# Performance work log

Measured on AMD Instinct MI355X. Metric: run time of the kernel, lower is better.

Reference implementation:

```python
import jax, jax.numpy as jnp
import numpy as np

B, T, ENC, DEC, ATTN = 64, 2048, 512, 512, 256


def setup_inputs() -> dict:
    key = jax.random.key(0)
    k1, k2, k3, k4, k5, k6 = jax.random.split(key, 6)
    enc_out = jax.random.normal(k1, (B, T, ENC), dtype=jnp.float32)
    dec_hidden = jax.random.normal(k2, (B, DEC), dtype=jnp.float32)
    mask = jax.random.randint(k3, (B, T), 0, 2) == 1  # True = masked out
    # learned params (Linear with bias=False); torch Linear weight is [out,in],
    # we store transposed [in,out] for x @ W convention
    s_enc = 1.0 / np.sqrt(ENC)
    s_dec = 1.0 / np.sqrt(DEC)
    s_v = 1.0 / np.sqrt(ATTN)
    W_enc = jax.random.uniform(k4, (ENC, ATTN), jnp.float32, -s_enc, s_enc)
    W_dec = jax.random.uniform(k5, (DEC, ATTN), jnp.float32, -s_dec, s_dec)
    v = jax.random.uniform(k6, (ATTN,), jnp.float32, -s_v, s_v)
    return {"enc_out": enc_out, "dec_hidden": dec_hidden, "mask": mask,
            "W_enc": W_enc, "W_dec": W_dec, "v": v}


def reference(enc_out, dec_hidden, mask, W_enc, W_dec, v):
    # proj_enc: [B,T,A]; proj_dec: [B,1,A]
    proj_enc = jnp.einsum('bte,ea->bta', enc_out, W_enc)
    proj_dec = jnp.einsum('bd,da->ba', dec_hidden, W_dec)[:, None, :]
    # energy: [B,T] -- additive (Bahdanau) score
    energy = jnp.einsum('bta,a->bt', jnp.tanh(proj_enc + proj_dec), v)
    energy = jnp.where(mask, -jnp.inf, energy)
    attn_w = jax.nn.softmax(energy, axis=-1)
    attn_w = jnp.nan_to_num(attn_w, nan=0.0)  # fully-masked rows -> 0
    context = jnp.einsum('bt,bte->be', attn_w, enc_out)
    return context, attn_w
```

## Files before the change

### kernel.cpp

```cpp
#include <hip/hip_runtime.h>
#include <stdint.h>

#define Bx 64
#define Tx 2048
#define ENCx 512
#define ATTx 256

typedef float f4 __attribute__((ext_vector_type(4)));
typedef float f32x4 __attribute__((ext_vector_type(4)));
typedef short bf16x8 __attribute__((ext_vector_type(8)));

__device__ __forceinline__ unsigned short f2bf(float f) {
  union { float f; uint32_t u; } c; c.f = f;
  uint32_t u = c.u;
  u += 0x7fffu + ((u >> 16) & 1u);
  return (unsigned short)(u >> 16);
}

__device__ __forceinline__ float ftanh(float x) {
  x = fminf(8.f, fmaxf(-8.f, x));
  float z = __expf(2.f * x);
  return 1.f - __fdividef(2.f, z + 1.f);
}

__global__ void k0_wt(const float* __restrict__ W, unsigned short* __restrict__ WTc) {
  int tid = blockIdx.x * 256 + threadIdx.x;
  int kc = tid >> 13;
  int r = tid & 8191;
  int n = r >> 5;
  int kk = r & 31;
  WTc[tid] = f2bf(W[(kc * 32 + kk) * ATTx + n]);
}

__global__ void k1_pd(const float* __restrict__ dec, const float* __restrict__ Wd,
                      float* __restrict__ pd) {
  __shared__ float ld[512];
  int b = blockIdx.x, a = threadIdx.x;
  ld[a] = dec[b * 512 + a];
  ld[a + 256] = dec[b * 512 + a + 256];
  __syncthreads();
  float s = 0.f;
#pragma unroll 8
  for (int d = 0; d < 512; ++d) s = fmaf(ld[d], Wd[d * ATTx + a], s);
  pd[b * ATTx + a] = s;
}

__global__ __launch_bounds__(256) void k2_energy(
    const float* __restrict__ enc, const unsigned short* __restrict__ WTc,
    const float* __restrict__ pd, const float* __restrict__ v,
    const int* __restrict__ mask, float* __restrict__ energy) {
  __shared__ unsigned short Alds[64 * 40];
  __shared__ unsigned short Wlds[256 * 40];
  __shared__ float ep[4][64];

  const int tid = threadIdx.x;
  const int wid = tid >> 6;
  const int lane = tid & 63;
  const int q = lane >> 4;
  const int c15 = lane & 15;
  const int m0 = blockIdx.x * 64;
  const int b = m0 >> 11;

  f32x4 acc[4][4];
#pragma unroll
  for (int i = 0; i < 4; ++i)
#pragma unroll
    for (int j = 0; j < 4; ++j) { f32x4 z = {0.f,0.f,0.f,0.f}; acc[i][j] = z; }

  const int ar = tid >> 2;
  const int ak = (tid & 3) * 8;
  const int wn = tid >> 2;
  const int wk = (tid & 3) * 8;

  for (int kc = 0; kc < 16; ++kc) {
    const f4* ap = (const f4*)(enc + (size_t)(m0 + ar) * ENCx + kc * 32 + ak);
    f4 a0 = ap[0];
    f4 a1 = ap[1];
    uint4 wv[4];
    const uint4* wp = (const uint4*)(WTc + kc * 8192);
#pragma unroll
    for (int it = 0; it < 4; ++it) wv[it] = wp[it * 256 + tid];

    if (kc) __syncthreads();

    union { unsigned short s[8]; uint4 u; } aw;
    aw.s[0] = f2bf(a0.x); aw.s[1] = f2bf(a0.y); aw.s[2] = f2bf(a0.z); aw.s[3] = f2bf(a0.w);
    aw.s[4] = f2bf(a1.x); aw.s[5] = f2bf(a1.y); aw.s[6] = f2bf(a1.z); aw.s[7] = f2bf(a1.w);
    *(uint4*)&Alds[ar * 40 + ak] = aw.u;
#pragma unroll
    for (int it = 0; it < 4; ++it)
      *(uint4*)&Wlds[(it * 64 + wn) * 40 + wk] = wv[it];
    __syncthreads();

    bf16x8 af[4], bfr[4];
#pragma unroll
    for (int rt = 0; rt < 4; ++rt)
      af[rt] = *(const bf16x8*)&Alds[(rt * 16 + c15) * 40 + q * 8];
#pragma unroll
    for (int ct = 0; ct < 4; ++ct)
      bfr[ct] = *(const bf16x8*)&Wlds[(wid * 64 + ct * 16 + c15) * 40 + q * 8];
#pragma unroll
    for (int rt = 0; rt < 4; ++rt)
#pragma unroll
      for (int ct = 0; ct < 4; ++ct)
        acc[rt][ct] = __builtin_amdgcn_mfma_f32_16x16x32_bf16(af[rt], bfr[ct], acc[rt][ct], 0, 0, 0);
  }

  float part[4][4];
#pragma unroll
  for (int rt = 0; rt < 4; ++rt)
#pragma unroll
    for (int i = 0; i < 4; ++i) part[rt][i] = 0.f;
#pragma unroll
  for (int ct = 0; ct < 4; ++ct) {
    int col = wid * 64 + ct * 16 + c15;
    float pdv = pd[b * ATTx + col];
    float vv = v[col];
#pragma unroll
    for (int rt = 0; rt < 4; ++rt)
#pragma unroll
      for (int i = 0; i < 4; ++i)
        part[rt][i] += ftanh(acc[rt][ct][i] + pdv) * vv;
  }
#pragma unroll
  for (int s = 1; s < 16; s <<= 1)
#pragma unroll
    for (int rt = 0; rt < 4; ++rt)
#pragma unroll
      for (int i = 0; i < 4; ++i)
        part[rt][i] += __shfl_xor(part[rt][i], s, 64);
  if (c15 == 0)
#pragma unroll
    for (int rt = 0; rt < 4; ++rt)
#pragma unroll
      for (int i = 0; i < 4; ++i)
        ep[wid][rt * 16 + q * 4 + i] = part[rt][i];
  __syncthreads();
  if (tid < 64) {
    float e = ep[0][tid] + ep[1][tid] + ep[2][tid] + ep[3][tid];
    int gm = m0 + tid;
    if (mask[gm]) e = -1e30f;
    energy[gm] = e;
  }
}

__global__ void k3_softmax(const float* __restrict__ energy, float* __restrict__ attn) {
  __shared__ float redm[4];
  __shared__ float redl[4];
  int b = blockIdx.x, tid = threadIdx.x;
  int lane = tid & 63, wid = tid >> 6;
  float e[8];
#pragma unroll
  for (int i = 0; i < 8; ++i) e[i] = energy[b * Tx + tid + i * 256];
  float m = e[0];
#pragma unroll
  for (int i = 1; i < 8; ++i) m = fmaxf(m, e[i]);
#pragma unroll
  for (int s = 1; s < 64; s <<= 1) m = fmaxf(m, __shfl_xor(m, s, 64));
  if (lane == 0) redm[wid] = m;
  __syncthreads();
  m = fmaxf(fmaxf(redm[0], redm[1]), fmaxf(redm[2], redm[3]));
  bool dead = (m < -1e29f);
  float w[8];
  float l = 0.f;
#pragma unroll
  for (int i = 0; i < 8; ++i) { w[i] = dead ? 0.f : __expf(e[i] - m); l += w[i]; }
#pragma unroll
  for (int s = 1; s < 64; s <<= 1) l += __shfl_xor(l, s, 64);
  if (lane == 0) redl[wid] = l;
  __syncthreads();
  l = redl[0] + redl[1] + redl[2] + redl[3];
  float inv = dead ? 0.f : __fdividef(1.f, l);
#pragma unroll
  for (int i = 0; i < 8; ++i) attn[b * Tx + tid + i * 256] = w[i] * inv;
}

__global__ void k4_ctx(const float* __restrict__ enc, const float* __restrict__ attn,
                       float* __restrict__ part) {
  __shared__ float wl[256];
  __shared__ f4 comb[128];
  int tc = blockIdx.x & 7, b = blockIdx.x >> 3;
  int tid = threadIdx.x;
  wl[tid] = attn[b * Tx + tc * 256 + tid];
  __syncthreads();
  int tl = tid >> 7;
  int ef = tid & 127;
  f4 a = {0.f, 0.f, 0.f, 0.f};
  const f4* base = (const f4*)(enc + ((size_t)b * Tx + tc * 256) * ENCx) + ef;
  for (int t = tl; t < 256; t += 2) {
    float wv = wl[t];
    f4 x = base[(size_t)t * 128];
    a += x * wv;
  }
  if (tl == 1) comb[ef] = a;
  __syncthreads();
  if (tl == 0) {
    a += comb[ef];
    *((f4*)(part + ((size_t)tc * 64 + b) * 512) + ef) = a;
  }
}

__global__ void k5_red(const float* __restrict__ part, float* __restrict__ ctx) {
  int idx = blockIdx.x * 256 + threadIdx.x;
  float s = 0.f;
#pragma unroll
  for (int tc = 0; tc < 8; ++tc) s += part[tc * 32768 + idx];
  ctx[idx] = s;
}

extern "C" void kernel_launch(void* const* d_in, const int* in_sizes, int n_in,
                              void* d_out, int out_size, void* d_ws, size_t ws_size,
                              hipStream_t stream) {
  const float* enc   = (const float*)d_in[0];
  const float* dec   = (const float*)d_in[1];
  const int*   mask  = (const int*)d_in[2];
  const float* W_enc = (const float*)d_in[3];
  const float* W_dec = (const float*)d_in[4];
  const float* v     = (const float*)d_in[5];
  float* ctx  = (float*)d_out;
  float* attn = ctx + Bx * ENCx;
  char* ws = (char*)d_ws;
  unsigned short* WTc = (unsigned short*)ws;
  float* pd     = (float*)(ws + 262144);
  float* energy = (float*)(ws + 262144 + 65536);
  float* part   = (float*)(ws + 262144 + 65536 + 524288);

  k0_wt<<<512, 256, 0, stream>>>(W_enc, WTc);
  k1_pd<<<64, 256, 0, stream>>>(dec, W_dec, pd);
  k2_energy<<<2048, 256, 0, stream>>>(enc, WTc, pd, v, mask, energy);
  k3_softmax<<<64, 256, 0, stream>>>(energy, attn);
  k4_ctx<<<512, 256, 0, stream>>>(enc, attn, part);
  k5_red<<<128, 256, 0, stream>>>(part, ctx);
}
```

Baseline: 577.9 us.

## Drop LDS staging in energy GEMM and split context reduction finer

The energy kernel now has each wave compute a 32-row by 256-column tile. A and W fragments are loaded straight from global memory into registers, with no LDS staging and no per-k-chunk barriers. It uses a cheaper packed bf16 conversion (round-half-up via perm), keeps pd/v in LDS, and writes masked energies directly without a cross-wave LDS reduction. The context kernel splits T into 16 chunks instead of 8 to launch more blocks, which doubles the partial sums the final reduce has to read. W is re-read from global/L2 by each wave, and the larger accumulator array raises register pressure.

```diff
diff --git a/kernel.cpp b/kernel.cpp
--- a/kernel.cpp
+++ b/kernel.cpp
@@ -15,6 +15,12 @@
   uint32_t u = c.u;
   u += 0x7fffu + ((u >> 16) & 1u);
   return (unsigned short)(u >> 16);
+}
+
+__device__ __forceinline__ uint32_t pk_bf(float lo, float hi) {
+  uint32_t a = __float_as_uint(lo) + 0x8000u;
+  uint32_t b = __float_as_uint(hi) + 0x8000u;
+  return __builtin_amdgcn_perm(b, a, 0x07060302u);
 }
 
 __device__ __forceinline__ float ftanh(float x) {
@@ -49,98 +55,85 @@
     const float* __restrict__ enc, const unsigned short* __restrict__ WTc,
     const float* __restrict__ pd, const float* __restrict__ v,
     const int* __restrict__ mask, float* __restrict__ energy) {
-  __shared__ unsigned short Alds[64 * 40];
-  __shared__ unsigned short Wlds[256 * 40];
-  __shared__ float ep[4][64];
-
+  __shared__ float pdv[256];
+  __shared__ float vvs[256];
   const int tid = threadIdx.x;
   const int wid = tid >> 6;
   const int lane = tid & 63;
   const int q = lane >> 4;
   const int c15 = lane & 15;
-  const int m0 = blockIdx.x * 64;
+  const int m0 = blockIdx.x * 128;
   const int b = m0 >> 11;
 
-  f32x4 acc[4][4];
-#pragma unroll
-  for (int i = 0; i < 4; ++i)
-#pragma unroll
-    for (int j = 0; j < 4; ++j) { f32x4 z = {0.f,0.f,0.f,0.f}; acc[i][j] = z; }
-
-  const int ar = tid >> 2;
-  const int ak = (tid & 3) * 8;
-  const int wn = tid >> 2;
-  const int wk = (tid & 3) * 8;
+  pdv[tid] = pd[b * ATTx + tid];
+  vvs[tid] = v[tid];
+  __syncthreads();
+
+  const int mrow = m0 + wid * 32 + c15;
+  const float* a0p = enc + (size_t)mrow * ENCx + q * 8;
+  const float* a1p = a0p + 16 * ENCx;
+  const unsigned short* wb = WTc + c15 * 32 + q * 8;
+
+  f32x4 acc[2][16];
+#pragma unroll
+  for (int mt = 0; mt < 2; ++mt)
+#pragma unroll
+    for (int ct = 0; ct < 16; ++ct) { f32x4 z = {0.f,0.f,0.f,0.f}; acc[mt][ct] = z; }
 
   for (int kc = 0; kc < 16; ++kc) {
-    const f4* ap = (const f4*)(enc + (size_t)(m0 + ar) * ENCx + kc * 32 + ak);
-    f4 a0 = ap[0];
-    f4 a1 = ap[1];
-    uint4 wv[4];
-    const uint4* wp = (const uint4*)(WTc + kc * 8192);
-#pragma unroll
-    for (int it = 0; it < 4; ++it) wv[it] = wp[it * 256 + tid];
-
-    if (kc) __syncthreads();
-
-    union { unsigned short s[8]; uint4 u; } aw;
-    aw.s[0] = f2bf(a0.x); aw.s[1] = f2bf(a0.y); aw.s[2] = f2bf(a0.z); aw.s[3] = f2bf(a0.w);
-    aw.s[4] = f2bf(a1.x); aw.s[5] = f2bf(a1.y); aw.s[6] = f2bf(a1.z); aw.s[7] = f2bf(a1.w);
-    *(uint4*)&Alds[ar * 40 + ak] = aw.u;
-#pragma unroll
-    for (int it = 0; it < 4; ++it)
-      *(uint4*)&Wlds[(it * 64 + wn) * 40 + wk] = wv[it];
-    __syncthreads();
-
-    bf16x8 af[4], bfr[4];
-#pragma unroll
-    for (int rt = 0; rt < 4; ++rt)
-      af[rt] = *(const bf16x8*)&Alds[(rt * 16 + c15) * 40 + q * 8];
-#pragma unroll
-    for (int ct = 0; ct < 4; ++ct)
-      bfr[ct] = *(const bf16x8*)&Wlds[(wid * 64 + ct * 16 + c15) * 40 + q * 8];
-#pragma unroll
-    for (int rt = 0; rt < 4; ++rt)
-#pragma unroll
-      for (int ct = 0; ct < 4; ++ct)
-        acc[rt][ct] = __builtin_amdgcn_mfma_f32_16x16x32_bf16(af[rt], bfr[ct], acc[rt][ct], 0, 0, 0);
-  }
-
-  float part[4][4];
-#pragma unroll
-  for (int rt = 0; rt < 4; ++rt)
-#pragma unroll
-    for (int i = 0; i < 4; ++i) part[rt][i] = 0.f;
-#pragma unroll
-  for (int ct = 0; ct < 4; ++ct) {
-    int col = wid * 64 + ct * 16 + c15;
-    float pdv = pd[b * ATTx + col];
-    float vv = v[col];
-#pragma unroll
-    for (int rt = 0; rt < 4; ++rt)
+    f4 x0 = *(const f4*)(a0p + kc * 32);
+    f4 x1 = *(const f4*)(a0p + kc * 32 + 4);
+    f4 y0 = *(const f4*)(a1p + kc * 32);
+    f4 y1 = *(const f4*)(a1p + kc * 32 + 4);
+    bf16x8 bfr[16];
+    const unsigned short* wkc = wb + kc * 8192;
+#pragma unroll
+    for (int ct = 0; ct < 16; ++ct)
+      bfr[ct] = *(const bf16x8*)(wkc + ct * 512);
+
+    union { uint32_t u[4]; bf16x8 v; } am0, am1;
+    am0.u[0] = pk_bf(x0.x, x0.y); am0.u[1] = pk_bf(x0.z, x0.w);
+    am0.u[2] = pk_bf(x1.x, x1.y); am0.u[3] = pk_bf(x1.z, x1.w);
+    am1.u[0] = pk_bf(y0.x, y0.y); am1.u[1] = pk_bf(y0.z, y0.w);
+    am1.u[2] = pk_bf(y1.x, y1.y); am1.u[3] = pk_bf(y1.z, y1.w);
+
+#pragma unroll
+    for (int ct = 0; ct < 16; ++ct) {
+      acc[0][ct] = __builtin_amdgcn_mfma_f32_16x16x32_bf16(am0.v, bfr[ct], acc[0][ct], 0, 0, 0);
+      acc[1][ct] = __builtin_amdgcn_mfma_f32_16x16x32_bf16(am1.v, bfr[ct], acc[1][ct], 0, 0, 0);
+    }
+  }
+
+  float ps[2][4];
+#pragma unroll
+  for (int mt = 0; mt < 2; ++mt)
+#pragma unroll
+    for (int i = 0; i < 4; ++i) ps[mt][i] = 0.f;
+#pragma unroll
+  for (int ct = 0; ct < 16; ++ct) {
+    float pv = pdv[ct * 16 + c15];
+    float vv = vvs[ct * 16 + c15];
+#pragma unroll
+    for (int mt = 0; mt < 2; ++mt)
 #pragma unroll
       for (int i = 0; i < 4; ++i)
-        part[rt][i] += ftanh(acc[rt][ct][i] + pdv) * vv;
+        ps[mt][i] += ftanh(acc[mt][ct][i] + pv) * vv;
   }
 #pragma unroll
   for (int s = 1; s < 16; s <<= 1)
 #pragma unroll
-    for (int rt = 0; rt < 4; ++rt)
+    for (int mt = 0; mt < 2; ++mt)
 #pragma unroll
       for (int i = 0; i < 4; ++i)
-        part[rt][i] += __shfl_xor(part[rt][i], s, 64);
-  if (c15 == 0)
-#pragma unroll
-    for (int rt = 0; rt < 4; ++rt)
-#pragma unroll
-      for (int i = 0; i < 4; ++i)
-        ep[wid][rt * 16 + q * 4 + i] = part[rt][i];
-  __syncthreads();
-  if (tid < 64) {
-    float e = ep[0][tid] + ep[1][tid] + ep[2][tid] + ep[3][tid];
-    int gm = m0 + tid;
-    if (mask[gm]) e = -1e30f;
-    energy[gm] = e;
+        ps[mt][i] += __shfl_xor(ps[mt][i], s, 64);
+  if (c15 == 0) {
+#pragma unroll
+    for (int mt = 0; mt < 2; ++mt)
+#pragma unroll
+      for (int i = 0; i < 4; ++i) {
+        int gm = m0 + wid * 32 + mt * 16 + q * 4 + i;
+        energy[gm] = mask[gm] ? -1e30f : ps[mt][i];
+      }
   }
 }
 
@@ -177,20 +170,19 @@
 
 __global__ void k4_ctx(const float* __restrict__ enc, const float* __restrict__ attn,
                        float* __restrict__ part) {
-  __shared__ float wl[256];
+  __shared__ float wl[128];
   __shared__ f4 comb[128];
-  int tc = blockIdx.x & 7, b = blockIdx.x >> 3;
+  int tc = blockIdx.x & 15, b = blockIdx.x >> 4;
   int tid = threadIdx.x;
-  wl[tid] = attn[b * Tx + tc * 256 + tid];
+  if (tid < 128) wl[tid] = attn[b * Tx + tc * 128 + tid];
   __syncthreads();
   int tl = tid >> 7;
   int ef = tid & 127;
   f4 a = {0.f, 0.f, 0.f, 0.f};
-  const f4* base = (const f4*)(enc + ((size_t)b * Tx + tc * 256) * ENCx) + ef;
-  for (int t = tl; t < 256; t += 2) {
-    float wv = wl[t];
+  const f4* base = (const f4*)(enc + ((size_t)b * Tx + tc * 128) * ENCx) + ef;
+  for (int t = tl; t < 128; t += 2) {
     f4 x = base[(size_t)t * 128];
-    a += x * wv;
+    a += x * wl[t];
   }
   if (tl == 1) comb[ef] = a;
   __syncthreads();
@@ -204,7 +196,7 @@
   int idx = blockIdx.x * 256 + threadIdx.x;
   float s = 0.f;
 #pragma unroll
-  for (int tc = 0; tc < 8; ++tc) s += part[tc * 32768 + idx];
+  for (int tc = 0; tc < 16; ++tc) s += part[tc * 32768 + idx];
   ctx[idx] = s;
 }
 
@@ -227,8 +219,8 @@
 
   k0_wt<<<512, 256, 0, stream>>>(W_enc, WTc);
   k1_pd<<<64, 256, 0, stream>>>(dec, W_dec, pd);
-  k2_energy<<<2048, 256, 0, stream>>>(enc, WTc, pd, v, mask, energy);
+  k2_energy<<<1024, 256, 0, stream>>>(enc, WTc, pd, v, mask, energy);
   k3_softmax<<<64, 256, 0, stream>>>(energy, attn);
-  k4_ctx<<<512, 256, 0, stream>>>(enc, attn, part);
+  k4_ctx<<<1024, 256, 0, stream>>>(enc, attn, part);
   k5_red<<<128, 256, 0, stream>>>(part, ctx);
 }
```

Result: faster. 488.0 us (-15.6%).
